# Kernel optimization log

Hardware: AMD Instinct MI355X
Metric: run time of the kernel (lower is better)

Reference implementation:

```python
import jax, jax.numpy as jnp
import numpy as np

B, IN_DIM, R_DIM = 8192, 2048, 4096
LEAK_RATE = 0.3


def setup_inputs() -> dict:
    key = jax.random.key(0)
    k1, k2, k3, k4 = jax.random.split(key, 4)
    inputs = jax.random.normal(k1, (B, IN_DIM), dtype=jnp.float32)
    prev_state = jax.random.normal(k2, (B, R_DIM), dtype=jnp.float32)
    # weights scaled down for numerical sanity inside tanh
    input_weights = jax.random.normal(k3, (R_DIM, IN_DIM), dtype=jnp.float32) * 0.02
    reservoir_weights = jax.random.normal(k4, (R_DIM, R_DIM), dtype=jnp.float32) * 0.02
    return {
        "inputs": inputs,
        "prev_state": prev_state,
        "input_weights": input_weights,
        "reservoir_weights": reservoir_weights,
    }


def reference(inputs, prev_state, input_weights, reservoir_weights):
    # input_part = inputs @ input_weights.T        -> [B, R]
    # reservoir_part = prev_state @ reservoir_weights.T -> [B, R]
    input_part = jnp.einsum("bi,ri->br", inputs, input_weights)
    reservoir_part = jnp.einsum("bq,rq->br", prev_state, reservoir_weights)
    state = (1.0 - LEAK_RATE) * prev_state + LEAK_RATE * jnp.tanh(input_part + reservoir_part)
    return state
```

## Files before the change

kernel.cpp:

```cpp
#include <hip/hip_runtime.h>
#include <cstdint>
#include <cstddef>

typedef unsigned short u16;
typedef __attribute__((ext_vector_type(8))) short short8;
typedef __attribute__((ext_vector_type(4))) float f32x4;
typedef __attribute__((ext_vector_type(4))) int i32x4;

constexpr int M  = 8192;
constexpr int Nn = 4096;
constexpr int K1 = 2048;
constexpr int K2 = 4096;
constexpr int K  = K1 + K2;
constexpr int BM = 256, BN = 256;
constexpr int NKT = K / 64;
constexpr float LEAK = 0.3f;

__device__ __forceinline__ u16 f2bf(float f) {
  unsigned u = __float_as_uint(f);
  u += 0x7FFFu + ((u >> 16) & 1u);
  return (u16)(u >> 16);
}

template<int C1, int C2>
__global__ void cast_concat(const float* __restrict__ X, const float* __restrict__ S,
                            u16* __restrict__ out, int rows)
{
  constexpr int C = C1 + C2;
  const size_t total = (size_t)rows * C / 8;
  for (size_t i = blockIdx.x * (size_t)blockDim.x + threadIdx.x; i < total;
       i += (size_t)gridDim.x * blockDim.x) {
    const size_t e = i * 8;
    const int r = (int)(e / C);
    const int c = (int)(e - (size_t)r * C);
    const float* src = (c < C1) ? (X + (size_t)r * C1 + c)
                                : (S + (size_t)r * C2 + (c - C1));
    const float4* s4 = (const float4*)src;
    float4 f0 = s4[0], f1 = s4[1];
    alignas(16) u16 tmp[8];
    tmp[0] = f2bf(f0.x); tmp[1] = f2bf(f0.y); tmp[2] = f2bf(f0.z); tmp[3] = f2bf(f0.w);
    tmp[4] = f2bf(f1.x); tmp[5] = f2bf(f1.y); tmp[6] = f2bf(f1.z); tmp[7] = f2bf(f1.w);
    *(i32x4*)(out + e) = *(i32x4*)tmp;
  }
}

__device__ __forceinline__ void gload16(const u16* g, u16* l) {
  __builtin_amdgcn_global_load_lds(
      (const __attribute__((address_space(1))) void*)g,
      (__attribute__((address_space(3))) void*)l, 16, 0, 0);
}

__device__ __forceinline__ float fast_tanh(float x) {
  const float ax = __builtin_fabsf(x);
  const float e  = __builtin_amdgcn_exp2f(ax * 2.8853900817779268f);
  const float r  = 1.0f - 2.0f * __builtin_amdgcn_rcpf(e + 1.0f);
  return __builtin_copysignf(r, x);
}

#define BAR()   __builtin_amdgcn_s_barrier()
#define LGKM0() asm volatile("s_waitcnt lgkmcnt(0)" ::: "memory")
#define LGKM4() asm volatile("s_waitcnt lgkmcnt(4)" ::: "memory")
#define LGKM8() asm volatile("s_waitcnt lgkmcnt(8)" ::: "memory")
#define VMW2()  asm volatile("s_waitcnt vmcnt(2)" ::: "memory")
#define VMW4()  asm volatile("s_waitcnt vmcnt(4)" ::: "memory")
#define VMW0()  asm volatile("s_waitcnt vmcnt(0)" ::: "memory")
#define SB0()   __builtin_amdgcn_sched_barrier(0)

__global__ __launch_bounds__(512, 2) void gemm_fused(
    const u16* __restrict__ A,
    const u16* __restrict__ W,
    const float* __restrict__ prev,
    float* __restrict__ out)
{
  __shared__ u16 lds[65536];

  const int tid  = threadIdx.x;
  const int lane = tid & 63;
  const int wid  = tid >> 6;
  const int wr   = wid >> 2;
  const int wc   = wid & 3;

  const int cpx = gridDim.x >> 3;
  const int wg  = ((int)blockIdx.x & 7) * cpx + ((int)blockIdx.x >> 3);
  const int bn  = wg & 15;
  const int bm  = wg >> 4;

  const int sr = tid >> 3;
  const int ss = (tid & 7) ^ (sr & 7);
  const u16* pA = A + (size_t)(bm * BM + sr) * K + ss * 8;
  const u16* pW = W + (size_t)(bn * BN + sr) * K + ss * 8;
  u16* ldsw = lds + wid * 512;
  const size_t rowK64  = (size_t)64  * K;
  const size_t rowK128 = (size_t)128 * K;

  auto stg = [&](const u16* g, int dst) {
    gload16(g,          ldsw + dst);
    gload16(g + rowK64, ldsw + dst + 4096);
  };

  const int fr  = lane & 15;
  const int khi = lane >> 4;
  const int lx  = lane & 7;
  const int aoff0 = wr * 8192 + fr * 64 + ((khi    ) ^ lx) * 8;
  const int aoff1 = wr * 8192 + fr * 64 + ((4 + khi) ^ lx) * 8;
  const int brow  = (wc & 1) * 64 + fr;
  const int boff0 = (wc >> 1) * 8192 + brow * 64 + ((khi    ) ^ lx) * 8;
  const int boff1 = (wc >> 1) * 8192 + brow * 64 + ((4 + khi) ^ lx) * 8;

  short8 afE[4][2], afO[4][2];
  short8 bfE[2][2], bfO[2][2];
  f32x4  acc[8][4];
  #pragma unroll
  for (int m = 0; m < 8; ++m)
    #pragma unroll
    for (int n = 0; n < 4; ++n) acc[m][n] = (f32x4)0.f;

  auto dsA = [&](short8 (&Av)[4][2], int mg, int ab) {
    #pragma unroll
    for (int mi = 0; mi < 4; ++mi) {
      Av[mi][0] = *(const short8*)(lds + ab + aoff0 + (mg * 4 + mi) * 1024);
      Av[mi][1] = *(const short8*)(lds + ab + aoff1 + (mg * 4 + mi) * 1024);
    }
  };
  auto dsB = [&](short8 (&Bv)[2][2], int ng, int bb) {
    #pragma unroll
    for (int ni = 0; ni < 2; ++ni) {
      Bv[ni][0] = *(const short8*)(lds + bb + boff0 + (ng * 2 + ni) * 1024);
      Bv[ni][1] = *(const short8*)(lds + bb + boff1 + (ng * 2 + ni) * 1024);
    }
  };
  auto MM = [&](short8 (&Av)[4][2], short8 (&Bv)[2][2], int mg, int ng) {
    __builtin_amdgcn_s_setprio(1);
    #pragma unroll
    for (int ni = 0; ni < 2; ++ni)
      #pragma unroll
      for (int mi = 0; mi < 4; ++mi)
        #pragma unroll
        for (int ks = 0; ks < 2; ++ks)
          acc[mg * 4 + mi][ng * 2 + ni] = __builtin_amdgcn_mfma_f32_16x16x32_bf16(
              Av[mi][ks], Bv[ni][ks], acc[mg * 4 + mi][ng * 2 + ni], 0, 0, 0);
    __builtin_amdgcn_s_setprio(0);
  };

  stg(pA,            0);
  stg(pA + rowK128,  8192);
  stg(pW,            32768);
  stg(pW + rowK128,  32768 + 8192);
  stg(pW + 64,       49152);
  stg(pA + 64,       16384);
  VMW4();
  BAR();
  dsA(afE, 0, 0);
  dsB(bfE, 0, 32768);

  const u16* gA = pA;
  const u16* gW = pW;
  #pragma unroll 1
  for (int i = 0; i < 47; ++i) {
    dsB(bfO, 1, 32768);
    stg(gA + 64 + rowK128, 16384 + 8192);
    LGKM4(); SB0(); MM(afE, bfE, 0, 0); BAR();
    dsA(afO, 1, 0);
    stg(gW + 64 + rowK128, 49152 + 8192);
    LGKM8(); SB0(); MM(afE, bfO, 0, 1); VMW2(); BAR();
    dsA(afE, 0, 16384);
    stg(gW + 128, 32768);
    LGKM8(); SB0(); MM(afO, bfE, 1, 0); VMW2(); BAR();
    dsB(bfE, 0, 49152);
    stg(gA + 128, 0);
    SB0(); MM(afO, bfO, 1, 1); BAR();
    dsB(bfO, 1, 49152);
    stg(gA + 128 + rowK128, 8192);
    LGKM4(); SB0(); MM(afE, bfE, 0, 0); BAR();
    dsA(afO, 1, 16384);
    stg(gW + 128 + rowK128, 32768 + 8192);
    LGKM8(); SB0(); MM(afE, bfO, 0, 1); VMW2(); BAR();
    dsA(afE, 0, 0);
    stg(gW + 192, 49152);
    LGKM8(); SB0(); MM(afO, bfE, 1, 0); VMW2(); BAR();
    dsB(bfE, 0, 32768);
    stg(gA + 192, 16384);
    SB0(); MM(afO, bfO, 1, 1); BAR();
    gA += 128; gW += 128;
  }

  dsB(bfO, 1, 32768);
  stg(gA + 64 + rowK128, 16384 + 8192);
  LGKM4(); SB0(); MM(afE, bfE, 0, 0); BAR();
  dsA(afO, 1, 0);
  stg(gW + 64 + rowK128, 49152 + 8192);
  LGKM8(); SB0(); MM(afE, bfO, 0, 1); VMW2(); BAR();
  dsA(afE, 0, 16384);
  LGKM8(); SB0(); MM(afO, bfE, 1, 0); VMW0(); BAR();
  dsB(bfE, 0, 49152);
  SB0(); MM(afO, bfO, 1, 1); BAR();
  dsB(bfO, 1, 49152);
  LGKM4(); SB0(); MM(afE, bfE, 0, 0); BAR();
  dsA(afO, 1, 16384);
  LGKM8(); SB0(); MM(afE, bfO, 0, 1); BAR();
  LGKM0(); SB0(); MM(afO, bfE, 1, 0);
  MM(afO, bfO, 1, 1);

  const int crow0 = bm * BM + wr * 128 + khi * 4;
  const int ccol0 = bn * BN + wc * 64 + fr;
  #pragma unroll
  for (int m = 0; m < 8; ++m)
    #pragma unroll
    for (int n = 0; n < 4; ++n)
      #pragma unroll
      for (int j = 0; j < 4; ++j) {
        const int row = crow0 + m * 16 + j;
        const size_t off = (size_t)row * Nn + ccol0 + n * 16;
        out[off] = (1.0f - LEAK) * prev[off] + LEAK * fast_tanh(acc[m][n][j]);
      }
}

extern "C" void kernel_launch(void* const* d_in, const int* in_sizes, int n_in,
                              void* d_out, int out_size, void* d_ws, size_t ws_size,
                              hipStream_t stream) {
  const float* inputs = (const float*)d_in[0];
  const float* prev   = (const float*)d_in[1];
  const float* w_in   = (const float*)d_in[2];
  const float* w_res  = (const float*)d_in[3];
  float* out = (float*)d_out;

  u16* Acat = (u16*)d_ws;
  u16* Wcat = Acat + (size_t)M * K;

  cast_concat<K1, K2><<<2048, 256, 0, stream>>>(inputs, prev, Acat, M);
  cast_concat<K1, K2><<<1024, 256, 0, stream>>>(w_in, w_res, Wcat, Nn);

  gemm_fused<<<(M / BM) * (Nn / BN), 512, 0, stream>>>(Acat, Wcat, prev, out);
}
```

Measured before the change: 431.3 us.

## Switch GEMM to 32x32x16 MFMA tiles and regroup global-to-LDS staging

Measured after the change: 465.8 us. 8.0% more time.

```diff
diff --git a/kernel.cpp b/kernel.cpp
--- a/kernel.cpp
+++ b/kernel.cpp
@@ -4,7 +4,7 @@
 
 typedef unsigned short u16;
 typedef __attribute__((ext_vector_type(8))) short short8;
-typedef __attribute__((ext_vector_type(4))) float f32x4;
+typedef __attribute__((ext_vector_type(16))) float f32x16;
 typedef __attribute__((ext_vector_type(4))) int i32x4;
 
 constexpr int M  = 8192;
@@ -61,8 +61,7 @@
 #define LGKM0() asm volatile("s_waitcnt lgkmcnt(0)" ::: "memory")
 #define LGKM4() asm volatile("s_waitcnt lgkmcnt(4)" ::: "memory")
 #define LGKM8() asm volatile("s_waitcnt lgkmcnt(8)" ::: "memory")
-#define VMW2()  asm volatile("s_waitcnt vmcnt(2)" ::: "memory")
-#define VMW4()  asm volatile("s_waitcnt vmcnt(4)" ::: "memory")
+#define VMW8()  asm volatile("s_waitcnt vmcnt(8)" ::: "memory")
 #define VMW0()  asm volatile("s_waitcnt vmcnt(0)" ::: "memory")
 #define SB0()   __builtin_amdgcn_sched_barrier(0)
 
@@ -98,57 +97,51 @@
     gload16(g + rowK64, ldsw + dst + 4096);
   };
 
-  const int fr  = lane & 15;
-  const int khi = lane >> 4;
-  const int lx  = lane & 7;
-  const int aoff0 = wr * 8192 + fr * 64 + ((khi    ) ^ lx) * 8;
-  const int aoff1 = wr * 8192 + fr * 64 + ((4 + khi) ^ lx) * 8;
-  const int brow  = (wc & 1) * 64 + fr;
-  const int boff0 = (wc >> 1) * 8192 + brow * 64 + ((khi    ) ^ lx) * 8;
-  const int boff1 = (wc >> 1) * 8192 + brow * 64 + ((4 + khi) ^ lx) * 8;
-
-  short8 afE[4][2], afO[4][2];
-  short8 bfE[2][2], bfO[2][2];
-  f32x4  acc[8][4];
+  const int l31 = lane & 31, l5 = lane >> 5, l7 = lane & 7;
+  int aoffk[4], boffk[4];
   #pragma unroll
-  for (int m = 0; m < 8; ++m)
-    #pragma unroll
-    for (int n = 0; n < 4; ++n) acc[m][n] = (f32x4)0.f;
-
-  auto dsA = [&](short8 (&Av)[4][2], int mg, int ab) {
-    #pragma unroll
-    for (int mi = 0; mi < 4; ++mi) {
-      Av[mi][0] = *(const short8*)(lds + ab + aoff0 + (mg * 4 + mi) * 1024);
-      Av[mi][1] = *(const short8*)(lds + ab + aoff1 + (mg * 4 + mi) * 1024);
-    }
-  };
-  auto dsB = [&](short8 (&Bv)[2][2], int ng, int bb) {
-    #pragma unroll
-    for (int ni = 0; ni < 2; ++ni) {
-      Bv[ni][0] = *(const short8*)(lds + bb + boff0 + (ng * 2 + ni) * 1024);
-      Bv[ni][1] = *(const short8*)(lds + bb + boff1 + (ng * 2 + ni) * 1024);
-    }
-  };
-  auto MM = [&](short8 (&Av)[4][2], short8 (&Bv)[2][2], int mg, int ng) {
+  for (int ks = 0; ks < 4; ++ks) {
+    const int sk = (ks * 2 + l5) ^ l7;
+    aoffk[ks] = (wr * 128 + l31) * 64 + sk * 8;
+    boffk[ks] = (wc * 64  + l31) * 64 + sk * 8;
+  }
+
+  short8 afE[2][4], afO[2][4];
+  short8 bfE[4],    bfO[4];
+  f32x16 acc[4][2];
+  #pragma unroll
+  for (int mt = 0; mt < 4; ++mt)
+    #pragma unroll
+    for (int ng = 0; ng < 2; ++ng) acc[mt][ng] = (f32x16)0.f;
+
+  auto dsA = [&](short8 (&Av)[2][4], int mg, int ab) {
+    #pragma unroll
+    for (int mtl = 0; mtl < 2; ++mtl)
+      #pragma unroll
+      for (int ks = 0; ks < 4; ++ks)
+        Av[mtl][ks] = *(const short8*)(lds + ab + mg * 4096 + mtl * 2048 + aoffk[ks]);
+  };
+  auto dsB = [&](short8 (&Bv)[4], int ng, int bb) {
+    #pragma unroll
+    for (int ks = 0; ks < 4; ++ks)
+      Bv[ks] = *(const short8*)(lds + bb + ng * 2048 + boffk[ks]);
+  };
+  auto MM = [&](short8 (&Av)[2][4], short8 (&Bv)[4], int mg, int ng) {
     __builtin_amdgcn_s_setprio(1);
     #pragma unroll
-    for (int ni = 0; ni < 2; ++ni)
+    for (int ks = 0; ks < 4; ++ks)
       #pragma unroll
-      for (int mi = 0; mi < 4; ++mi)
-        #pragma unroll
-        for (int ks = 0; ks < 2; ++ks)
-          acc[mg * 4 + mi][ng * 2 + ni] = __builtin_amdgcn_mfma_f32_16x16x32_bf16(
-              Av[mi][ks], Bv[ni][ks], acc[mg * 4 + mi][ng * 2 + ni], 0, 0, 0);
+      for (int mtl = 0; mtl < 2; ++mtl)
+        acc[mg * 2 + mtl][ng] = __builtin_amdgcn_mfma_f32_32x32x16_bf16(
+            Av[mtl][ks], Bv[ks], acc[mg * 2 + mtl][ng], 0, 0, 0);
     __builtin_amdgcn_s_setprio(0);
   };
 
-  stg(pA,            0);
-  stg(pA + rowK128,  8192);
-  stg(pW,            32768);
-  stg(pW + rowK128,  32768 + 8192);
-  stg(pW + 64,       49152);
-  stg(pA + 64,       16384);
-  VMW4();
+  stg(pW,                 32768); stg(pW + rowK128,      32768 + 8192);
+  stg(pA,                 0);     stg(pA + rowK128,      8192);
+  stg(pW + 64,            49152); stg(pW + 64 + rowK128, 49152 + 8192);
+  stg(pA + 64,            16384); stg(pA + 64 + rowK128, 16384 + 8192);
+  VMW8();
   BAR();
   dsA(afE, 0, 0);
   dsB(bfE, 0, 32768);
@@ -158,40 +151,34 @@
   #pragma unroll 1
   for (int i = 0; i < 47; ++i) {
     dsB(bfO, 1, 32768);
-    stg(gA + 64 + rowK128, 16384 + 8192);
     LGKM4(); SB0(); MM(afE, bfE, 0, 0); BAR();
     dsA(afO, 1, 0);
-    stg(gW + 64 + rowK128, 49152 + 8192);
-    LGKM8(); SB0(); MM(afE, bfO, 0, 1); VMW2(); BAR();
+    LGKM8(); SB0(); MM(afE, bfO, 0, 1); VMW0(); BAR();
     dsA(afE, 0, 16384);
-    stg(gW + 128, 32768);
-    LGKM8(); SB0(); MM(afO, bfE, 1, 0); VMW2(); BAR();
+    stg(gW + 128, 32768); stg(gW + 128 + rowK128, 32768 + 8192);
+    LGKM8(); SB0(); MM(afO, bfE, 1, 0); BAR();
     dsB(bfE, 0, 49152);
-    stg(gA + 128, 0);
+    stg(gA + 128, 0); stg(gA + 128 + rowK128, 8192);
     SB0(); MM(afO, bfO, 1, 1); BAR();
     dsB(bfO, 1, 49152);
-    stg(gA + 128 + rowK128, 8192);
     LGKM4(); SB0(); MM(afE, bfE, 0, 0); BAR();
     dsA(afO, 1, 16384);
-    stg(gW + 128 + rowK128, 32768 + 8192);
-    LGKM8(); SB0(); MM(afE, bfO, 0, 1); VMW2(); BAR();
+    LGKM8(); SB0(); MM(afE, bfO, 0, 1); VMW0(); BAR();
     dsA(afE, 0, 0);
-    stg(gW + 192, 49152);
-    LGKM8(); SB0(); MM(afO, bfE, 1, 0); VMW2(); BAR();
+    stg(gW + 192, 49152); stg(gW + 192 + rowK128, 49152 + 8192);
+    LGKM8(); SB0(); MM(afO, bfE, 1, 0); BAR();
     dsB(bfE, 0, 32768);
-    stg(gA + 192, 16384);
+    stg(gA + 192, 16384); stg(gA + 192 + rowK128, 16384 + 8192);
     SB0(); MM(afO, bfO, 1, 1); BAR();
     gA += 128; gW += 128;
   }
 
   dsB(bfO, 1, 32768);
-  stg(gA + 64 + rowK128, 16384 + 8192);
   LGKM4(); SB0(); MM(afE, bfE, 0, 0); BAR();
   dsA(afO, 1, 0);
-  stg(gW + 64 + rowK128, 49152 + 8192);
-  LGKM8(); SB0(); MM(afE, bfO, 0, 1); VMW2(); BAR();
+  LGKM8(); SB0(); MM(afE, bfO, 0, 1); VMW0(); BAR();
   dsA(afE, 0, 16384);
-  LGKM8(); SB0(); MM(afO, bfE, 1, 0); VMW0(); BAR();
+  LGKM8(); SB0(); MM(afO, bfE, 1, 0); BAR();
   dsB(bfE, 0, 49152);
   SB0(); MM(afO, bfO, 1, 1); BAR();
   dsB(bfO, 1, 49152);
@@ -201,17 +188,17 @@
   LGKM0(); SB0(); MM(afO, bfE, 1, 0);
   MM(afO, bfO, 1, 1);
 
-  const int crow0 = bm * BM + wr * 128 + khi * 4;
-  const int ccol0 = bn * BN + wc * 64 + fr;
+  const int crow0 = bm * BM + wr * 128 + l5 * 4;
+  const int ccol0 = bn * BN + wc * 64 + l31;
   #pragma unroll
-  for (int m = 0; m < 8; ++m)
-    #pragma unroll
-    for (int n = 0; n < 4; ++n)
+  for (int mt = 0; mt < 4; ++mt)
+    #pragma unroll
+    for (int ng = 0; ng < 2; ++ng)
       #pragma unroll
-      for (int j = 0; j < 4; ++j) {
-        const int row = crow0 + m * 16 + j;
-        const size_t off = (size_t)row * Nn + ccol0 + n * 16;
-        out[off] = (1.0f - LEAK) * prev[off] + LEAK * fast_tanh(acc[m][n][j]);
+      for (int j = 0; j < 16; ++j) {
+        const int row = crow0 + mt * 32 + (j & 3) + 8 * (j >> 2);
+        const size_t off = (size_t)row * Nn + ccol0 + ng * 32;
+        out[off] = (1.0f - LEAK) * prev[off] + LEAK * fast_tanh(acc[mt][ng][j]);
       }
 }
 
```
